# Performance work log

Hardware: AMD Instinct MI355X
Metric: run time of the kernel (lower is better)

Reference implementation:

```python
import jax, jax.numpy as jnp
import numpy as np

VOCAB = 32000
D_IN = 1024      # == 2 * N_OUT so highway uses raw x (k=3 SRU path)
N_OUT = 512      # hidden per direction
N_LAYERS = 4
L, B = 1024, 16


def _sru_bidir_layer(x, W, b, n):
    """x: (L,B,2n), W: (2n, 6n) [dir0: xt,f,r | dir1: xt,f,r], b: (4n,) = [bf(2n), br(2n)]."""
    u = jnp.einsum('lbd,dk->lbk', x, W)  # (L,B,6n)
    bf, br = b[:2 * n], b[2 * n:]
    hs, cs = [], []
    for d, rev in ((0, False), (1, True)):
        ud = u[..., d * 3 * n:(d + 1) * 3 * n]
        xt = ud[..., :n]
        f = jax.nn.sigmoid(ud[..., n:2 * n] + bf[d * n:(d + 1) * n])
        r = jax.nn.sigmoid(ud[..., 2 * n:3 * n] + br[d * n:(d + 1) * n])
        xp = x[..., d * n:(d + 1) * n]  # highway input (k=3 case)

        def step(c, inp):
            xt_t, f_t, r_t, xp_t = inp
            c = f_t * c + (1.0 - f_t) * xt_t
            h = r_t * jnp.tanh(c) + (1.0 - r_t) * xp_t
            return c, h

        c0 = jnp.zeros((x.shape[1], n), x.dtype)
        c_last, h = jax.lax.scan(step, c0, (xt, f, r, xp), reverse=rev)
        hs.append(h)
        cs.append(c_last)
    return jnp.concatenate(hs, -1), jnp.concatenate(cs, -1)


def setup_inputs() -> dict:
    key = jax.random.key(0)
    k1, k2, k3, k4 = jax.random.split(key, 4)
    rnn_input = jax.random.randint(k1, (L, B), 0, VOCAB, dtype=jnp.int32)
    input_lengths = jax.random.randint(k2, (B,), 1, L + 1, dtype=jnp.int32)
    emb = jax.random.normal(k3, (VOCAB, D_IN), dtype=jnp.float32) * 0.05
    scale = 1.0 / np.sqrt(D_IN)
    Ws = jax.random.normal(k4, (N_LAYERS, D_IN, 6 * N_OUT), dtype=jnp.float32) * scale
    bs = jnp.zeros((N_LAYERS, 4 * N_OUT), dtype=jnp.float32)
    return {"rnn_input": rnn_input, "input_lengths": input_lengths,
            "emb": emb, "Ws": Ws, "bs": bs}


def reference(rnn_input, input_lengths, emb, Ws, bs):
    # input_lengths is unused in the original forward (no packing applied to SRU input)
    n = Ws.shape[-1] // 6
    x = emb[rnn_input]  # (L,B,D_IN)
    c_finals = []
    for l in range(Ws.shape[0]):
        x, c = _sru_bidir_layer(x, Ws[l], bs[l], n)
        c_finals.append(c)
    hidden = jnp.stack(c_finals, 0)  # (N_LAYERS, B, 2n)
    return x, hidden
```

## Files before the change

kernel.cpp:

```cpp
#include <hip/hip_runtime.h>
#include <hip/hip_bf16.h>
#include <cmath>

#define L_SEQ  1024
#define BATCH  16
#define NOUT   512
#define DIN    1024
#define NBIG   3072
#define NLAYERS 4
#define NTOK   (L_SEQ * BATCH)
#define NCHAIN 16384
#define SEG    32
#define SEGLEN (L_SEQ / SEG)

typedef __attribute__((ext_vector_type(8))) short bf16x8;
typedef __attribute__((ext_vector_type(4))) float f32x4;

__device__ __forceinline__ unsigned short f2bf(float f) {
    unsigned x = __float_as_uint(f);
    unsigned r = (x + 0x7fffu + ((x >> 16) & 1u)) >> 16;
    return (unsigned short)r;
}
__device__ __forceinline__ float bf2f(unsigned short hv) {
    return __uint_as_float((unsigned)hv << 16);
}
__device__ __forceinline__ float sigmf(float v) {
    return 1.f / (1.f + __expf(-v));
}
__device__ __forceinline__ void async16(const void* g, const void* l) {
    __builtin_amdgcn_global_load_lds(
        (const __attribute__((address_space(1))) unsigned int*)g,
        (__attribute__((address_space(3))) unsigned int*)l, 16, 0, 0);
}

__global__ __launch_bounds__(256)
void transpose_w(const float* __restrict__ Ws, unsigned short* __restrict__ Wt) {
    __shared__ float tile[32][33];
    int l = blockIdx.z;
    const float* W = Ws + (size_t)l * DIN * NBIG;
    unsigned short* Wo = Wt + (size_t)l * NBIG * DIN;
    int n0 = blockIdx.x * 32, k0 = blockIdx.y * 32;
    int tx = threadIdx.x & 31, ty = threadIdx.x >> 5;
    #pragma unroll
    for (int i = 0; i < 4; i++)
        tile[ty + 8 * i][tx] = W[(size_t)(k0 + ty + 8 * i) * NBIG + n0 + tx];
    __syncthreads();
    #pragma unroll
    for (int i = 0; i < 4; i++)
        Wo[(size_t)(n0 + ty + 8 * i) * DIN + k0 + tx] = f2bf(tile[tx][ty + 8 * i]);
}

__global__ void embed_kernel(const int* __restrict__ tok,
                             const float* __restrict__ emb,
                             float* __restrict__ x,
                             unsigned short* __restrict__ xbf) {
    int t = blockIdx.x;
    int row = tok[t];
    float4 v = ((const float4*)(emb + (size_t)row * DIN))[threadIdx.x];
    ((float4*)(x + (size_t)t * DIN))[threadIdx.x] = v;
    ushort4 h;
    h.x = f2bf(v.x); h.y = f2bf(v.y); h.z = f2bf(v.z); h.w = f2bf(v.w);
    ((ushort4*)(xbf + (size_t)t * DIN))[threadIdx.x] = h;
}


#define STAGE_A(b, mh, kt, src)                                             \
    do {                                                                    \
        _Pragma("unroll")                                                   \
        for (int q = 0; q < 2; q++) {                                       \
            int rbase = q * 128 + (mh) * 64 + w * 8;                        \
            async16((src) + (size_t)(rbase + sr) * DIN + (kt) * 64 + sc * 8,\
                    &lds[b][0][rbase * 64]);                                \
        }                                                                   \
    } while (0)

#define STAGE_B(b, nh, kt, src)                                             \
    do {                                                                    \
        _Pragma("unroll")                                                   \
        for (int q = 0; q < 2; q++) {                                       \
            int gi = q * 8 + w;                                             \
            int rbase = (gi >> 2) * 64 + (nh) * 32 + (gi & 3) * 8;          \
            async16((src) + (size_t)(rbase + sr) * DIN + (kt) * 64 + sc * 8,\
                    &lds[b][1][rbase * 64]);                                \
        }                                                                   \
    } while (0)

#define LOAD_A(b, mh)                                                       \
    do {                                                                    \
        _Pragma("unroll")                                                   \
        for (int i = 0; i < 4; i++) {                                       \
            int ra = wm * 128 + (mh) * 64 + i * 16 + l16;                   \
            _Pragma("unroll")                                               \
            for (int kk = 0; kk < 2; kk++) {                                \
                int slot = (kk * 4 + quad) ^ (ra & 7);                      \
                af[i][kk] = *(const bf16x8*)&lds[b][0][ra * 64 + slot * 8]; \
            }                                                               \
        }                                                                   \
    } while (0)

#define LOAD_B(b, nh)                                                       \
    do {                                                                    \
        _Pragma("unroll")                                                   \
        for (int j = 0; j < 2; j++) {                                       \
            int rb = wn * 64 + (nh) * 32 + j * 16 + l16;                    \
            _Pragma("unroll")                                               \
            for (int kk = 0; kk < 2; kk++) {                                \
                int slot = (kk * 4 + quad) ^ (rb & 7);                      \
                bg[j][kk] = *(const bf16x8*)&lds[b][1][rb * 64 + slot * 8]; \
            }                                                               \
        }                                                                   \
    } while (0)

#define MMA(mh, nh)                                                         \
    do {                                                                    \
        __builtin_amdgcn_s_setprio(1);                                      \
        _Pragma("unroll")                                                   \
        for (int i = 0; i < 4; i++)                                         \
            _Pragma("unroll")                                               \
            for (int j = 0; j < 2; j++)                                     \
                _Pragma("unroll")                                           \
                for (int kk = 0; kk < 2; kk++)                              \
                    acc[(mh) * 4 + i][(nh) * 2 + j] =                       \
                        __builtin_amdgcn_mfma_f32_16x16x32_bf16(            \
                            af[i][kk], bg[j][kk],                           \
                            acc[(mh) * 4 + i][(nh) * 2 + j], 0, 0, 0);      \
        __builtin_amdgcn_s_setprio(0);                                      \
    } while (0)

#define BAR()   __builtin_amdgcn_s_barrier()
#define LGKM0() do { asm volatile("s_waitcnt lgkmcnt(0)" ::: "memory");     \
                     __builtin_amdgcn_sched_barrier(0); } while (0)
#define LGKM8() asm volatile("s_waitcnt lgkmcnt(8)" ::: "memory")
#define VM6()   asm volatile("s_waitcnt vmcnt(6)" ::: "memory")
#define VM0()   asm volatile("s_waitcnt vmcnt(0)" ::: "memory")

__global__ __launch_bounds__(512)
void gemm_bf16(const unsigned short* __restrict__ Abf,
               const unsigned short* __restrict__ Bt,
               unsigned short* __restrict__ u_xt,
               unsigned short* __restrict__ u_f,
               unsigned short* __restrict__ u_r) {
    __shared__ __align__(16) unsigned short lds[2][2][256 * 64];

    const int tid  = threadIdx.x;
    const int lane = tid & 63;
    const int w    = tid >> 6;
    const int wm   = w >> 2, wn = w & 3;
    const int quad = lane >> 4, l16 = lane & 15;

    const int flat = blockIdx.y * (NBIG / 256) + blockIdx.x;
    const int swz  = (flat & 7) * (NTOK / 256 * NBIG / 256 / 8) + (flat >> 3);
    const int M0 = (swz / (NBIG / 256)) * 256;
    const int N0 = (swz % (NBIG / 256)) * 256;

    const unsigned short* Asrc = Abf + (size_t)M0 * DIN;
    const unsigned short* Bsrc = Bt  + (size_t)N0 * DIN;

    f32x4 acc[8][4];
    #pragma unroll
    for (int i = 0; i < 8; i++)
        #pragma unroll
        for (int j = 0; j < 4; j++)
            acc[i][j] = (f32x4){0.f, 0.f, 0.f, 0.f};

    const int sr = lane >> 3;
    const int sc = (lane & 7) ^ sr;

    bf16x8 af[4][2], bg[2][2];

    STAGE_A(0, 0, 0, Asrc); STAGE_B(0, 0, 0, Bsrc);
    STAGE_B(0, 1, 0, Bsrc); STAGE_A(0, 1, 0, Asrc);
    STAGE_A(1, 0, 1, Asrc); STAGE_B(1, 1, 1, Bsrc); STAGE_A(1, 1, 1, Asrc);
    VM6();
    BAR();

    const int NITER = DIN / 128;
    for (int t = 0; t < NITER; t++) {
        const int k1 = 2 * t + 1;
        const bool more = (t < NITER - 1);

        LOAD_A(0, 0); LOAD_B(0, 0);
        STAGE_B(1, 0, k1, Bsrc);
        LGKM8(); BAR(); LGKM0(); MMA(0, 0); BAR();
        LOAD_B(0, 1);
        if (more) STAGE_A(0, 0, k1 + 1, Asrc);
        BAR(); LGKM0(); MMA(0, 1); BAR();
        LOAD_A(0, 1);
        if (more) STAGE_B(0, 1, k1 + 1, Bsrc);
        BAR(); LGKM0(); MMA(1, 1); BAR();
        LOAD_B(0, 0);
        if (more) { STAGE_A(0, 1, k1 + 1, Asrc); VM6(); }
        else      { VM0(); }
        BAR(); LGKM0(); MMA(1, 0); BAR();

        LOAD_A(1, 0); LOAD_B(1, 0);
        if (more) STAGE_B(0, 0, k1 + 1, Bsrc);
        LGKM8(); BAR(); LGKM0(); MMA(0, 0); BAR();
        LOAD_B(1, 1);
        if (more) STAGE_A(1, 0, k1 + 2, Asrc);
        BAR(); LGKM0(); MMA(0, 1); BAR();
        LOAD_A(1, 1);
        if (more) STAGE_B(1, 1, k1 + 2, Bsrc);
        BAR(); LGKM0(); MMA(1, 1); BAR();
        LOAD_B(1, 0);
        if (more) { STAGE_A(1, 1, k1 + 2, Asrc); VM6(); }
        BAR(); LGKM0(); MMA(1, 0); BAR();
    }

    #pragma unroll
    for (int i = 0; i < 8; i++) {
        int gm = M0 + wm * 128 + i * 16 + quad * 4;
        #pragma unroll
        for (int j = 0; j < 4; j++) {
            int gn = N0 + wn * 64 + j * 16 + l16;
            int dir  = gn >= 3 * NOUT;
            int jj   = gn - dir * 3 * NOUT;
            int plane = jj >> 9;
            int feat  = jj & 511;
            unsigned short* p = (plane == 0 ? u_xt : plane == 1 ? u_f : u_r)
                                + (size_t)gm * DIN + dir * NOUT + feat;
            #pragma unroll
            for (int r = 0; r < 4; r++) p[(size_t)r * DIN] = f2bf(acc[i][j][r]);
        }
    }
}


__global__ __launch_bounds__(256)
void scan_phaseA(const unsigned short* __restrict__ u_xt, const unsigned short* __restrict__ u_f,
                 const float* __restrict__ bias,
                 float* __restrict__ Aseg, float* __restrict__ Bseg) {
    int g = blockIdx.x * 256 + threadIdx.x;
    int chain = g & (NCHAIN - 1);
    int s = g >> 14;
    int rest = chain & 1023;
    float bf = bias[rest];

    int d = rest >> 9;
    int t0 = d ? (L_SEQ - 1 - s * SEGLEN) : (s * SEGLEN);
    int sgn = d ? -1 : 1;
    long long idx = (long long)t0 * NCHAIN + chain;
    long long step = (long long)sgn * NCHAIN;

    float c = 0.f, A = 1.f;
    #pragma unroll 8
    for (int j = 0; j < SEGLEN; j++) {
        float xt = bf2f(u_xt[idx]);
        float f = sigmf(bf2f(u_f[idx]) + bf);
        c = f * c + (1.f - f) * xt;
        A *= f;
        idx += step;
    }
    Aseg[g] = A;
    Bseg[g] = c;
}

__global__ __launch_bounds__(256)
void scan_phaseB(const float* __restrict__ Aseg, const float* __restrict__ Bseg,
                 float* __restrict__ cstart, float* __restrict__ c_out) {
    int chain = blockIdx.x * 256 + threadIdx.x;
    float c = 0.f;
    #pragma unroll
    for (int s = 0; s < SEG; s++) {
        int g = s * NCHAIN + chain;
        cstart[g] = c;
        c = Aseg[g] * c + Bseg[g];
    }
    c_out[chain] = c;
}

__global__ __launch_bounds__(256)
void scan_phaseC(const unsigned short* __restrict__ u_xt, const unsigned short* __restrict__ u_f,
                 const unsigned short* __restrict__ u_r,
                 float* __restrict__ x, unsigned short* __restrict__ xbf,
                 const float* __restrict__ bias, const float* __restrict__ cstart,
                 int write_bf) {
    int g = blockIdx.x * 256 + threadIdx.x;
    int chain = g & (NCHAIN - 1);
    int s = g >> 14;
    int rest = chain & 1023;
    float bf = bias[rest];
    float br = bias[1024 + rest];

    int d = rest >> 9;
    int t0 = d ? (L_SEQ - 1 - s * SEGLEN) : (s * SEGLEN);
    int sgn = d ? -1 : 1;
    long long idx = (long long)t0 * NCHAIN + chain;
    long long step = (long long)sgn * NCHAIN;

    float c = cstart[g];
    #pragma unroll 4
    for (int j = 0; j < SEGLEN; j++) {
        float xt = bf2f(u_xt[idx]);
        float f = sigmf(bf2f(u_f[idx]) + bf);
        float r = sigmf(bf2f(u_r[idx]) + br);
        float xp = x[idx];
        c = f * c + (1.f - f) * xt;
        float th = 1.f - 2.f / (__expf(2.f * c) + 1.f);
        float h = r * th + (1.f - r) * xp;
        x[idx] = h;
        if (write_bf) xbf[idx] = f2bf(h);
        idx += step;
    }
}

extern "C" void kernel_launch(void* const* d_in, const int* in_sizes, int n_in,
                              void* d_out, int out_size, void* d_ws, size_t ws_size,
                              hipStream_t stream) {
    const int*   tok = (const int*)d_in[0];
    const float* emb = (const float*)d_in[2];
    const float* Ws  = (const float*)d_in[3];
    const float* bs  = (const float*)d_in[4];

    float* out    = (float*)d_out;
    float* x      = out;
    float* hidden = out + (size_t)NTOK * DIN;

    char* ws = (char*)d_ws;
    unsigned short* u_xt   = (unsigned short*)ws;
    unsigned short* u_f    = (unsigned short*)(ws + (32u  << 20));
    unsigned short* u_r    = (unsigned short*)(ws + (64u  << 20));
    unsigned short* xbf    = (unsigned short*)(ws + (96u  << 20));
    unsigned short* Wt     = (unsigned short*)(ws + (128u << 20));
    float*          Aseg   = (float*)(ws + (152u << 20));
    float*          Bseg   = (float*)(ws + (154u << 20));
    float*          cstart = (float*)(ws + (156u << 20));

    transpose_w<<<dim3(NBIG / 32, DIN / 32, NLAYERS), 256, 0, stream>>>(Ws, Wt);
    embed_kernel<<<NTOK, 256, 0, stream>>>(tok, emb, x, xbf);

    const int scan_blocks = NCHAIN * SEG / 256;

    for (int l = 0; l < NLAYERS; l++) {
        const unsigned short* Wl = Wt + (size_t)l * NBIG * DIN;
        const float* b = bs + (size_t)l * 4 * NOUT;
        gemm_bf16<<<dim3(NBIG / 256, NTOK / 256), 512, 0, stream>>>(xbf, Wl, u_xt, u_f, u_r);
        scan_phaseA<<<scan_blocks, 256, 0, stream>>>(u_xt, u_f, b, Aseg, Bseg);
        scan_phaseB<<<NCHAIN / 256, 256, 0, stream>>>(Aseg, Bseg, cstart,
                                                      hidden + (size_t)l * BATCH * DIN);
        scan_phaseC<<<scan_blocks, 256, 0, stream>>>(u_xt, u_f, u_r, x, xbf, b, cstart,
                                                     l < NLAYERS - 1);
    }
}
```

Baseline: 923.2 us.

## Make GEMM persistent over three N tiles with LDS-staged coalesced epilogue

The GEMM grid shrinks from 768 to 256 workgroups, each looping over three consecutive N tiles of the same M block with an XCD-aware mapping. The output epilogue goes through LDS, so each thread writes 16-byte coalesced chunks instead of scattered 2-byte stores, and the previous tile's global stores overlap with the next tile's prologue loads. B fragments are double-buffered per nh half so redundant LDS reloads can be dropped, and launch bounds request two workgroups per CU. This adds register pressure from the ctmp buffer and extra barriers, and the fewer, longer workgroups can leave some CUs idle at the tail.

```diff
diff --git a/kernel.cpp b/kernel.cpp
--- a/kernel.cpp
+++ b/kernel.cpp
@@ -106,7 +106,7 @@
             _Pragma("unroll")                                               \
             for (int kk = 0; kk < 2; kk++) {                                \
                 int slot = (kk * 4 + quad) ^ (rb & 7);                      \
-                bg[j][kk] = *(const bf16x8*)&lds[b][1][rb * 64 + slot * 8]; \
+                bg[nh][j][kk] = *(const bf16x8*)&lds[b][1][rb * 64 + slot * 8]; \
             }                                                               \
         }                                                                   \
     } while (0)
@@ -122,25 +122,54 @@
                 for (int kk = 0; kk < 2; kk++)                              \
                     acc[(mh) * 4 + i][(nh) * 2 + j] =                       \
                         __builtin_amdgcn_mfma_f32_16x16x32_bf16(            \
-                            af[i][kk], bg[j][kk],                           \
+                            af[i][kk], bg[nh][j][kk],                       \
                             acc[(mh) * 4 + i][(nh) * 2 + j], 0, 0, 0);      \
         __builtin_amdgcn_s_setprio(0);                                      \
     } while (0)
 
-#define BAR()   __builtin_amdgcn_s_barrier()
-#define LGKM0() do { asm volatile("s_waitcnt lgkmcnt(0)" ::: "memory");     \
-                     __builtin_amdgcn_sched_barrier(0); } while (0)
-#define LGKM8() asm volatile("s_waitcnt lgkmcnt(8)" ::: "memory")
-#define VM6()   asm volatile("s_waitcnt vmcnt(6)" ::: "memory")
-#define VM0()   asm volatile("s_waitcnt vmcnt(0)" ::: "memory")
-
-__global__ __launch_bounds__(512)
+#define BAR()    __builtin_amdgcn_s_barrier()
+#define LGKM0()  do { asm volatile("s_waitcnt lgkmcnt(0)" ::: "memory");    \
+                      __builtin_amdgcn_sched_barrier(0); } while (0)
+#define LGKM8()  asm volatile("s_waitcnt lgkmcnt(8)" ::: "memory")
+#define VM6()    asm volatile("s_waitcnt vmcnt(6)" ::: "memory")
+#define VM0()    asm volatile("s_waitcnt vmcnt(0)" ::: "memory")
+#define VM22()   asm volatile("s_waitcnt vmcnt(22)" ::: "memory")
+
+#define ZERO_ACC()                                                          \
+    do { _Pragma("unroll") for (int i = 0; i < 8; i++)                      \
+         _Pragma("unroll") for (int j = 0; j < 4; j++)                      \
+             acc[i][j] = (f32x4){0.f, 0.f, 0.f, 0.f}; } while (0)
+
+#define EP_DSWRITE()                                                        \
+    do { _Pragma("unroll") for (int i = 0; i < 8; i++)                      \
+         _Pragma("unroll") for (int j = 0; j < 4; j++)                      \
+         _Pragma("unroll") for (int r = 0; r < 4; r++) {                    \
+             int row = wm * 128 + i * 16 + quad * 4 + r;                    \
+             int ft  = (wn * 64 + j * 16 + l16) ^ (quad << 4);              \
+             Cbuf[row * 256 + ft] = f2bf(acc[i][j][r]);                     \
+         } } while (0)
+
+#define EP_READ()                                                           \
+    do { _Pragma("unroll") for (int ps = 0; ps < 16; ps++) {                \
+             int cg = ps * 512 + tid; int row = cg >> 5; int c0 = cg & 31;  \
+             int st = row * 256 + ((c0 << 3) ^ (((row >> 2) & 3) << 4));    \
+             ctmp[ps] = *(const bf16x8*)&Cbuf[st];                          \
+         } } while (0)
+
+#define EP_STORE(PL)                                                        \
+    do { _Pragma("unroll") for (int ps = 0; ps < 16; ps++) {                \
+             int cg = ps * 512 + tid; int row = cg >> 5; int c0 = cg & 31;  \
+             *(bf16x8*)((PL) + (size_t)(M0 + row) * DIN + c0 * 8) = ctmp[ps]; \
+         } } while (0)
+
+__global__ __launch_bounds__(512, 2)
 void gemm_bf16(const unsigned short* __restrict__ Abf,
                const unsigned short* __restrict__ Bt,
                unsigned short* __restrict__ u_xt,
                unsigned short* __restrict__ u_f,
                unsigned short* __restrict__ u_r) {
     __shared__ __align__(16) unsigned short lds[2][2][256 * 64];
+    unsigned short* Cbuf = &lds[0][0][0];
 
     const int tid  = threadIdx.x;
     const int lane = tid & 63;
@@ -148,81 +177,96 @@
     const int wm   = w >> 2, wn = w & 3;
     const int quad = lane >> 4, l16 = lane & 15;
 
-    const int flat = blockIdx.y * (NBIG / 256) + blockIdx.x;
-    const int swz  = (flat & 7) * (NTOK / 256 * NBIG / 256 / 8) + (flat >> 3);
-    const int M0 = (swz / (NBIG / 256)) * 256;
-    const int N0 = (swz % (NBIG / 256)) * 256;
+    const int bid = blockIdx.x;
+    const int xcd = bid & 7;
+    const int k   = bid >> 3;
+    const int M0  = (xcd * 8 + (k >> 2)) * 256;
+    const int p3  = (k & 3) * 3;
 
     const unsigned short* Asrc = Abf + (size_t)M0 * DIN;
-    const unsigned short* Bsrc = Bt  + (size_t)N0 * DIN;
 
     f32x4 acc[8][4];
-    #pragma unroll
-    for (int i = 0; i < 8; i++)
-        #pragma unroll
-        for (int j = 0; j < 4; j++)
-            acc[i][j] = (f32x4){0.f, 0.f, 0.f, 0.f};
+    bf16x8 af[4][2], bg[2][2][2];
+    bf16x8 ctmp[16];
 
     const int sr = lane >> 3;
     const int sc = (lane & 7) ^ sr;
 
-    bf16x8 af[4][2], bg[2][2];
-
-    STAGE_A(0, 0, 0, Asrc); STAGE_B(0, 0, 0, Bsrc);
-    STAGE_B(0, 1, 0, Bsrc); STAGE_A(0, 1, 0, Asrc);
-    STAGE_A(1, 0, 1, Asrc); STAGE_B(1, 1, 1, Bsrc); STAGE_A(1, 1, 1, Asrc);
-    VM6();
+    unsigned short* prev_pl = nullptr;
+
+    #pragma unroll 1
+    for (int c = 0; c < 3; c++) {
+        const int N0 = (p3 + c) * 256;
+        const unsigned short* Bsrc = Bt + (size_t)N0 * DIN;
+        const int dir = N0 >= 3 * NOUT;
+        const int jj0 = N0 - dir * 3 * NOUT;
+        const int plane = jj0 >> 9;
+        unsigned short* pl = (plane == 0 ? u_xt : plane == 1 ? u_f : u_r)
+                             + dir * NOUT + (jj0 & 511);
+
+        if (c == 0) {
+            ZERO_ACC();
+            STAGE_A(0, 0, 0, Asrc); STAGE_B(0, 0, 0, Bsrc);
+            STAGE_B(0, 1, 0, Bsrc); STAGE_A(0, 1, 0, Asrc);
+            STAGE_A(1, 0, 1, Asrc); STAGE_B(1, 1, 1, Bsrc); STAGE_A(1, 1, 1, Asrc);
+            VM6();
+            BAR();
+        } else {
+            EP_DSWRITE();
+            asm volatile("s_waitcnt lgkmcnt(0)" ::: "memory");
+            ZERO_ACC();
+            BAR();
+            EP_READ();
+            LGKM0();
+            BAR();
+            STAGE_A(0, 0, 0, Asrc); STAGE_B(0, 0, 0, Bsrc);
+            STAGE_B(0, 1, 0, Bsrc); STAGE_A(0, 1, 0, Asrc);
+            STAGE_A(1, 0, 1, Asrc); STAGE_B(1, 1, 1, Bsrc); STAGE_A(1, 1, 1, Asrc);
+            EP_STORE(prev_pl);
+            VM22();
+            BAR();
+        }
+
+        const int NITER = DIN / 128;
+        for (int t = 0; t < NITER; t++) {
+            const int k1 = 2 * t + 1;
+            const bool more = (t < NITER - 1);
+
+            LOAD_A(0, 0); LOAD_B(0, 0);
+            STAGE_B(1, 0, k1, Bsrc);
+            LGKM8(); BAR(); LGKM0(); MMA(0, 0); BAR();
+            LOAD_B(0, 1);
+            if (more) STAGE_A(0, 0, k1 + 1, Asrc);
+            BAR(); LGKM0(); MMA(0, 1); BAR();
+            LOAD_A(0, 1);
+            if (more) STAGE_B(0, 1, k1 + 1, Bsrc);
+            BAR(); LGKM0(); MMA(1, 1); BAR();
+            if (more) { STAGE_A(0, 1, k1 + 1, Asrc); VM6(); }
+            else      { VM0(); }
+            BAR(); MMA(1, 0); BAR();
+
+            LOAD_A(1, 0); LOAD_B(1, 0);
+            if (more) STAGE_B(0, 0, k1 + 1, Bsrc);
+            LGKM8(); BAR(); LGKM0(); MMA(0, 0); BAR();
+            LOAD_B(1, 1);
+            if (more) STAGE_A(1, 0, k1 + 2, Asrc);
+            BAR(); LGKM0(); MMA(0, 1); BAR();
+            LOAD_A(1, 1);
+            if (more) STAGE_B(1, 1, k1 + 2, Bsrc);
+            BAR(); LGKM0(); MMA(1, 1); BAR();
+            if (more) { STAGE_A(1, 1, k1 + 2, Asrc); VM6(); }
+            BAR(); MMA(1, 0); BAR();
+        }
+
+        prev_pl = pl;
+    }
+
+    EP_DSWRITE();
+    asm volatile("s_waitcnt lgkmcnt(0)" ::: "memory");
     BAR();
-
-    const int NITER = DIN / 128;
-    for (int t = 0; t < NITER; t++) {
-        const int k1 = 2 * t + 1;
-        const bool more = (t < NITER - 1);
-
-        LOAD_A(0, 0); LOAD_B(0, 0);
-        STAGE_B(1, 0, k1, Bsrc);
-        LGKM8(); BAR(); LGKM0(); MMA(0, 0); BAR();
-        LOAD_B(0, 1);
-        if (more) STAGE_A(0, 0, k1 + 1, Asrc);
-        BAR(); LGKM0(); MMA(0, 1); BAR();
-        LOAD_A(0, 1);
-        if (more) STAGE_B(0, 1, k1 + 1, Bsrc);
-        BAR(); LGKM0(); MMA(1, 1); BAR();
-        LOAD_B(0, 0);
-        if (more) { STAGE_A(0, 1, k1 + 1, Asrc); VM6(); }
-        else      { VM0(); }
-        BAR(); LGKM0(); MMA(1, 0); BAR();
-
-        LOAD_A(1, 0); LOAD_B(1, 0);
-        if (more) STAGE_B(0, 0, k1 + 1, Bsrc);
-        LGKM8(); BAR(); LGKM0(); MMA(0, 0); BAR();
-        LOAD_B(1, 1);
-        if (more) STAGE_A(1, 0, k1 + 2, Asrc);
-        BAR(); LGKM0(); MMA(0, 1); BAR();
-        LOAD_A(1, 1);
-        if (more) STAGE_B(1, 1, k1 + 2, Bsrc);
-        BAR(); LGKM0(); MMA(1, 1); BAR();
-        LOAD_B(1, 0);
-        if (more) { STAGE_A(1, 1, k1 + 2, Asrc); VM6(); }
-        BAR(); LGKM0(); MMA(1, 0); BAR();
-    }
-
-    #pragma unroll
-    for (int i = 0; i < 8; i++) {
-        int gm = M0 + wm * 128 + i * 16 + quad * 4;
-        #pragma unroll
-        for (int j = 0; j < 4; j++) {
-            int gn = N0 + wn * 64 + j * 16 + l16;
-            int dir  = gn >= 3 * NOUT;
-            int jj   = gn - dir * 3 * NOUT;
-            int plane = jj >> 9;
-            int feat  = jj & 511;
-            unsigned short* p = (plane == 0 ? u_xt : plane == 1 ? u_f : u_r)
-                                + (size_t)gm * DIN + dir * NOUT + feat;
-            #pragma unroll
-            for (int r = 0; r < 4; r++) p[(size_t)r * DIN] = f2bf(acc[i][j][r]);
-        }
-    }
+    EP_READ();
+    LGKM0();
+    EP_STORE(prev_pl);
 }
 
 
@@ -334,7 +378,7 @@
     for (int l = 0; l < NLAYERS; l++) {
         const unsigned short* Wl = Wt + (size_t)l * NBIG * DIN;
         const float* b = bs + (size_t)l * 4 * NOUT;
-        gemm_bf16<<<dim3(NBIG / 256, NTOK / 256), 512, 0, stream>>>(xbf, Wl, u_xt, u_f, u_r);
+        gemm_bf16<<<256, 512, 0, stream>>>(xbf, Wl, u_xt, u_f, u_r);
         scan_phaseA<<<scan_blocks, 256, 0, stream>>>(u_xt, u_f, b, Aseg, Bseg);
         scan_phaseB<<<NCHAIN / 256, 256, 0, stream>>>(Aseg, Bseg, cstart,
                                                       hidden + (size_t)l * BATCH * DIN);
```

After: 1.199 ms. +29.9%, slower.
